# Kernel optimization log

Hardware: AMD Instinct MI355X
Metric: run time of the kernel (lower is better)

Reference implementation:

```python
import jax, jax.numpy as jnp
import numpy as np

N, NFEAT, NHID, NCLASS = 10000, 512, 64, 10
ALPHA = 0.2


def setup_inputs() -> dict:
    key = jax.random.key(0)
    ks = jax.random.split(key, 8)
    x = jax.random.normal(ks[0], (N, NFEAT), dtype=jnp.float32)
    adj1 = jax.random.uniform(ks[1], (N, N), dtype=jnp.float32) / N  # row-normalized-ish
    adj2 = jax.random.uniform(ks[2], (N, N), dtype=jnp.float32) / N
    # GraphConvolution params (glorot-ish scale)
    W1 = jax.random.normal(ks[3], (NFEAT, NHID), dtype=jnp.float32) * (1.0 / np.sqrt(NFEAT))
    b1 = jnp.zeros((NHID,), dtype=jnp.float32)
    W2 = jax.random.normal(ks[4], (NFEAT, NHID), dtype=jnp.float32) * (1.0 / np.sqrt(NFEAT))
    b2 = jnp.zeros((NHID,), dtype=jnp.float32)
    attn_w = jax.random.normal(ks[5], (NHID, 1), dtype=jnp.float32) * (1.0 / np.sqrt(NHID))
    cluster = jax.random.normal(ks[6], (NCLASS, NHID), dtype=jnp.float32)
    return {"x": x, "adj1": adj1, "adj2": adj2, "W1": W1, "b1": b1,
            "W2": W2, "b2": b2, "attn_w": attn_w, "cluster": cluster}


def reference(x, adj1, adj2, W1, b1, W2, b2, attn_w, cluster):
    # Two GCN branches: output = adj @ (x @ W) + b
    emb1 = adj1 @ (x @ W1) + b1  # [N, H]
    emb2 = adj2 @ (x @ W2) + b2  # [N, H]
    z = jnp.stack([emb1, emb2], axis=1)            # [N, 2, H]
    # tiny 2-way attention fusion
    w = z @ attn_w                                  # [N, 2, 1]
    beta = jax.nn.softmax(w, axis=1)                # softmax over the 2 views
    emb = jnp.sum(beta * z, axis=1)                 # [N, H]
    # DEC cluster assignment (faithful to the original, including the
    # second power and the /2, which the row-normalization cancels)
    d2 = jnp.sum((emb[:, None, :] - cluster[None, :, :]) ** 2, axis=2)  # [N, K]
    q = 1.0 / (1.0 + d2 / ALPHA)
    q = q ** ((ALPHA + 1.0) / 2.0)
    q = q ** (ALPHA + 1.0) / 2.0
    q = q / jnp.sum(q, axis=1, keepdims=True)
    return emb, q
```

## Files before the change

kernel.cpp:

```cpp
#include <hip/hip_runtime.h>
#include <math.h>

#define NROWS 10000
#define FEAT  512
#define NHID  64
#define NCLS  10
#define YT_STRIDE 10240
#define KB_PAD 320
#define TK    128
#define NSPLIT 8
#define TILES_PER_SPLIT 10

typedef __attribute__((ext_vector_type(8))) short short8;
typedef __attribute__((ext_vector_type(4))) float f32x4;

__device__ __forceinline__ short f2bf(float f) {
  union { float f; unsigned u; } v; v.f = f;
  unsigned r = v.u + 0x7fffu + ((v.u >> 16) & 1u);
  return (short)(r >> 16);
}

__device__ __forceinline__ float wsum64(float v) {
#pragma unroll
  for (int off = 32; off > 0; off >>= 1) v += __shfl_xor(v, off, 64);
  return v;
}

__device__ __forceinline__ void gload16(const void* g, void* l) {
  __builtin_amdgcn_global_load_lds(
      (const __attribute__((address_space(1))) unsigned int*)g,
      (__attribute__((address_space(3))) unsigned int*)l, 16, 0, 0);
}

__global__ __launch_bounds__(256) void prep_w(const float* __restrict__ W1,
                                              const float* __restrict__ W2,
                                              unsigned short* __restrict__ Wt1,
                                              unsigned short* __restrict__ Wt2) {
  int i = blockIdx.x * 256 + threadIdx.x;
  if (i >= FEAT * NHID) return;
  int k = i >> 6, h = i & 63;
  Wt1[h * FEAT + k] = (unsigned short)f2bf(W1[i]);
  Wt2[h * FEAT + k] = (unsigned short)f2bf(W2[i]);
}

__global__ __launch_bounds__(256) void gemm_xw(const float* __restrict__ x,
                                               const unsigned short* __restrict__ Wt1,
                                               const unsigned short* __restrict__ Wt2,
                                               unsigned short* __restrict__ Yt1,
                                               unsigned short* __restrict__ Yt2) {
  const int lane = threadIdx.x & 63;
  const int wave = threadIdx.x >> 6;
  const int job = blockIdx.x * 4 + wave;
  if (job >= 1250) return;
  const int br = (job >= 625) ? 1 : 0;
  const int tile = job - 625 * br;
  const unsigned short* Wt = br ? Wt2 : Wt1;
  unsigned short* Yt       = br ? Yt2 : Yt1;
  const int rowbase = tile * 16;
  const int r16 = lane & 15, g = lane >> 4, ga = g * 8;

  const float* arow = x + (size_t)(rowbase + r16) * FEAT + ga;
  const unsigned short* bp = Wt + (size_t)r16 * FEAT + ga;

  f32x4 acc[4];
#pragma unroll
  for (int t = 0; t < 4; ++t) acc[t] = (f32x4){0.f, 0.f, 0.f, 0.f};

#pragma unroll
  for (int kb = 0; kb < FEAT / 32; ++kb) {
    const int k0 = kb * 32;
    const f32x4* ap = (const f32x4*)(arow + k0);
    f32x4 a0 = ap[0], a1 = ap[1];
    short8 af;
    af[0] = f2bf(a0[0]); af[1] = f2bf(a0[1]); af[2] = f2bf(a0[2]); af[3] = f2bf(a0[3]);
    af[4] = f2bf(a1[0]); af[5] = f2bf(a1[1]); af[6] = f2bf(a1[2]); af[7] = f2bf(a1[3]);
#pragma unroll
    for (int t = 0; t < 4; ++t) {
      short8 bf = *(const short8*)(bp + (size_t)t * 16 * FEAT + k0);
      acc[t] = __builtin_amdgcn_mfma_f32_16x16x32_bf16(af, bf, acc[t], 0, 0, 0);
    }
  }
  const int sw = (r16 & 7) << 3;
#pragma unroll
  for (int t = 0; t < 4; ++t)
#pragma unroll
    for (int rr = 0; rr < 4; ++rr) {
      const int col = t * 16 + r16;
      const int row = rowbase + g * 4 + rr;
      Yt[(size_t)col * YT_STRIDE + (row ^ sw)] = (unsigned short)f2bf(acc[t][rr]);
    }
}

__global__ __launch_bounds__(256, 4) void gemm_adj(const float* __restrict__ adj1,
                                                   const float* __restrict__ adj2,
                                                   const unsigned short* __restrict__ Yt1,
                                                   const unsigned short* __restrict__ Yt2,
                                                   float* __restrict__ Ep) {
  __shared__ __attribute__((aligned(16))) float Asm[2][32 * TK];

  const int sp = blockIdx.y;
  const int br = blockIdx.z;
  const float* adj         = br ? adj2 : adj1;
  const unsigned short* Yt = br ? Yt2 : Yt1;
  float* E = Ep + (size_t)(br * NSPLIT + sp) * NROWS * NHID;
  const int k_base = sp * (TILES_PER_SPLIT * TK);
  const int blockrow = blockIdx.x * 32;

  const int lane = threadIdx.x & 63;
  const int wave = threadIdx.x >> 6;

  const int l32 = lane >> 5;
  const int a_lin = (lane & 31) * 4;

  const int wr = wave >> 1, wc = wave & 1;
  const int r16 = lane & 15, g = lane >> 4;
  const int arow_t = wr * 16 + r16;
  const int aswz = (arow_t & 7) << 2;
  const int swb = (r16 & 7) << 3;

  const int colL = wc * 32 + r16;
  const unsigned short* ytL = Yt + (size_t)colL * YT_STRIDE;
  const unsigned short* ytH = ytL + (size_t)16 * YT_STRIDE;

  f32x4 accL = (f32x4){0.f, 0.f, 0.f, 0.f};
  f32x4 accH = accL;

#define STAGE_A(tt) { const int k0s = k_base + (tt) * TK; const int bufs = (tt) & 1; \
    _Pragma("unroll")                                                                 \
    for (int j = 0; j < 4; ++j) {                                                     \
      const int rt = wave * 8 + 2 * j + l32;                                          \
      const int gr = min(blockrow + rt, NROWS - 1);                                   \
      const int fsrc = a_lin ^ ((rt & 7) << 2);                                       \
      const float* asrc = adj + (size_t)gr * NROWS + min(k0s + fsrc, NROWS - 4);      \
      gload16(asrc, &Asm[bufs][(wave * 8 + 2 * j) * TK]);                             \
    } }

#define BLOAD(tt) { const int k0b = k_base + (tt) * TK;                               \
    _Pragma("unroll")                                                                 \
    for (int s = 0; s < 4; ++s) {                                                     \
      const int off = k0b + ((s * 32 + g * 8) ^ swb);                                 \
      BL[s] = *(const short8*)(ytL + off);                                            \
      BH[s] = *(const short8*)(ytH + off);                                            \
    } }

#define COMPUTE(tt) { const int bufc = (tt) & 1;                                      \
    const float* abase = &Asm[bufc][arow_t * TK];                                     \
    _Pragma("unroll")                                                                 \
    for (int s = 0; s < 4; ++s) {                                                     \
      const int kx = s * 32 + g * 8;                                                  \
      f32x4 a0 = *(const f32x4*)(abase + (kx ^ aswz));                                \
      f32x4 a1 = *(const f32x4*)(abase + ((kx + 4) ^ aswz));                          \
      short8 af;                                                                      \
      af[0] = f2bf(a0[0]); af[1] = f2bf(a0[1]); af[2] = f2bf(a0[2]); af[3] = f2bf(a0[3]); \
      af[4] = f2bf(a1[0]); af[5] = f2bf(a1[1]); af[6] = f2bf(a1[2]); af[7] = f2bf(a1[3]); \
      accL = __builtin_amdgcn_mfma_f32_16x16x32_bf16(af, BL[s], accL, 0, 0, 0);       \
      accH = __builtin_amdgcn_mfma_f32_16x16x32_bf16(af, BH[s], accH, 0, 0, 0);       \
    } }

  STAGE_A(0);
#pragma unroll 1
  for (int t = 0; t < TILES_PER_SPLIT - 1; ++t) {
    short8 BL[4], BH[4];
    BLOAD(t);
    __builtin_amdgcn_sched_barrier(0);
    asm volatile("" ::: "memory");
    STAGE_A(t + 1);
    asm volatile("s_waitcnt vmcnt(4)" ::: "memory");
    __builtin_amdgcn_sched_barrier(0);
    __builtin_amdgcn_s_barrier();
    __builtin_amdgcn_sched_barrier(0);
    COMPUTE(t);
    __builtin_amdgcn_s_barrier();
  }
  {
    short8 BL[4], BH[4];
    BLOAD(TILES_PER_SPLIT - 1);
    asm volatile("s_waitcnt vmcnt(0)" ::: "memory");
    __builtin_amdgcn_sched_barrier(0);
    __builtin_amdgcn_s_barrier();
    __builtin_amdgcn_sched_barrier(0);
    COMPUTE(TILES_PER_SPLIT - 1);
  }
#undef STAGE_A
#undef BLOAD
#undef COMPUTE

#pragma unroll
  for (int rr = 0; rr < 4; ++rr) {
    const int grow = blockrow + wr * 16 + g * 4 + rr;
    if (grow < NROWS) {
      float* e = E + (size_t)grow * NHID + wc * 32 + r16;
      e[0]  = accL[rr];
      e[16] = accH[rr];
    }
  }
}

__global__ __launch_bounds__(256) void gemm_adj_dyn(const float* __restrict__ adj1,
                                                    const float* __restrict__ adj2,
                                                    const unsigned short* __restrict__ Yt1,
                                                    const unsigned short* __restrict__ Yt2,
                                                    float* __restrict__ Ep,
                                                    int nsplit, int chunk) {
  const int sp = blockIdx.y;
  const int br = blockIdx.z;
  const float* adj          = br ? adj2 : adj1;
  const unsigned short* Yt  = br ? Yt2 : Yt1;
  float* E = Ep + (size_t)(br * nsplit + sp) * NROWS * NHID;

  const int kb_begin = sp * chunk;
  const int kb_end   = min(kb_begin + chunk, KB_PAD);

  const int lane = threadIdx.x & 63;
  const int wave = threadIdx.x >> 6;
  const int rowbase = blockIdx.x * 64 + wave * 16;
  if (rowbase >= NROWS) return;
  const int r = lane & 15;
  const int g = lane >> 4;
  const int ga = g * 8;
  const int sw = (r & 7) << 3;

  const float* arow = adj + (size_t)(rowbase + r) * NROWS;

  f32x4 acc0 = (f32x4){0.f, 0.f, 0.f, 0.f};
  f32x4 acc1 = acc0, acc2 = acc0, acc3 = acc0;

#pragma unroll 4
  for (int kb = kb_begin; kb < kb_end; ++kb) {
    const int k0 = kb * 32;
    const int kc = min(k0 + ga, 9992);
    const int ks = (k0 + ga) ^ sw;
    const f32x4* ap = (const f32x4*)(arow + kc);
    f32x4 a0 = ap[0], a1 = ap[1];
    short8 af;
    af[0] = f2bf(a0[0]); af[1] = f2bf(a0[1]); af[2] = f2bf(a0[2]); af[3] = f2bf(a0[3]);
    af[4] = f2bf(a1[0]); af[5] = f2bf(a1[1]); af[6] = f2bf(a1[2]); af[7] = f2bf(a1[3]);
    short8 bf0 = *(const short8*)(Yt + (size_t)(0 * 16 + r) * YT_STRIDE + ks);
    short8 bf1 = *(const short8*)(Yt + (size_t)(1 * 16 + r) * YT_STRIDE + ks);
    short8 bf2 = *(const short8*)(Yt + (size_t)(2 * 16 + r) * YT_STRIDE + ks);
    short8 bf3 = *(const short8*)(Yt + (size_t)(3 * 16 + r) * YT_STRIDE + ks);
    acc0 = __builtin_amdgcn_mfma_f32_16x16x32_bf16(af, bf0, acc0, 0, 0, 0);
    acc1 = __builtin_amdgcn_mfma_f32_16x16x32_bf16(af, bf1, acc1, 0, 0, 0);
    acc2 = __builtin_amdgcn_mfma_f32_16x16x32_bf16(af, bf2, acc2, 0, 0, 0);
    acc3 = __builtin_amdgcn_mfma_f32_16x16x32_bf16(af, bf3, acc3, 0, 0, 0);
  }

  const size_t ebase = (size_t)(rowbase + g * 4) * NHID + r;
#pragma unroll
  for (int rr = 0; rr < 4; ++rr) {
    E[ebase + (size_t)rr * NHID +  0] = acc0[rr];
    E[ebase + (size_t)rr * NHID + 16] = acc1[rr];
    E[ebase + (size_t)rr * NHID + 32] = acc2[rr];
    E[ebase + (size_t)rr * NHID + 48] = acc3[rr];
  }
}

__global__ __launch_bounds__(256) void fuse(const float* __restrict__ Ep,
                                            int nsplit,
                                            const float* __restrict__ b1,
                                            const float* __restrict__ b2,
                                            const float* __restrict__ aw,
                                            const float* __restrict__ cl,
                                            float* __restrict__ out) {
  const int lane = threadIdx.x & 63;
  const int wave = threadIdx.x >> 6;
  const int row = blockIdx.x * 4 + wave;
  if (row >= NROWS) return;

  const size_t off = (size_t)row * NHID + lane;
  const size_t bstride = (size_t)nsplit * NROWS * NHID;
  float e1 = b1[lane], e2 = b2[lane];
  for (int s = 0; s < nsplit; ++s) {
    e1 += Ep[(size_t)s * NROWS * NHID + off];
    e2 += Ep[bstride + (size_t)s * NROWS * NHID + off];
  }

  float a = aw[lane];
  float w1 = wsum64(e1 * a);
  float w2 = wsum64(e2 * a);
  float m = fmaxf(w1, w2);
  float x1 = expf(w1 - m), x2 = expf(w2 - m);
  float inv = 1.0f / (x1 + x2);
  float emb = (x1 * e1 + x2 * e2) * inv;
  out[off] = emb;

  float myq = 0.f, qs = 0.f;
#pragma unroll
  for (int c = 0; c < NCLS; ++c) {
    float d = emb - cl[c * NHID + lane];
    float s = wsum64(d * d);
    float t = exp2f(-0.72f * log2f(fmaf(5.0f, s, 1.0f)));
    qs += t;
    if (lane == c) myq = t;
  }
  if (lane < NCLS) out[(size_t)NROWS * NHID + (size_t)row * NCLS + lane] = myq / qs;
}

extern "C" void kernel_launch(void* const* d_in, const int* in_sizes, int n_in,
                              void* d_out, int out_size, void* d_ws, size_t ws_size,
                              hipStream_t stream) {
  const float* x    = (const float*)d_in[0];
  const float* adj1 = (const float*)d_in[1];
  const float* adj2 = (const float*)d_in[2];
  const float* W1   = (const float*)d_in[3];
  const float* b1   = (const float*)d_in[4];
  const float* W2   = (const float*)d_in[5];
  const float* b2   = (const float*)d_in[6];
  const float* aw   = (const float*)d_in[7];
  const float* cl   = (const float*)d_in[8];
  float* out = (float*)d_out;

  char* ws = (char*)d_ws;
  unsigned short* Yt1 = (unsigned short*)(ws + 0);
  unsigned short* Yt2 = (unsigned short*)(ws + 1310720);
  unsigned short* Wt1 = (unsigned short*)(ws + 2621440);
  unsigned short* Wt2 = (unsigned short*)(ws + 2686976);
  float* Ep           = (float*)(ws + 2752512);

  const size_t fixed = 2752512;
  const size_t per_split = 2ull * NROWS * NHID * 4ull;
  const bool static_ok = ws_size >= fixed + (size_t)NSPLIT * per_split;

  hipMemsetAsync(Yt1, 0, 2 * 1310720, stream);
  prep_w<<<dim3(128), dim3(256), 0, stream>>>(W1, W2, Wt1, Wt2);
  gemm_xw<<<dim3(313), dim3(256), 0, stream>>>(x, Wt1, Wt2, Yt1, Yt2);

  if (static_ok) {
    gemm_adj<<<dim3(313, NSPLIT, 2), dim3(256), 0, stream>>>(adj1, adj2, Yt1, Yt2, Ep);
    fuse<<<dim3(2500), dim3(256), 0, stream>>>(Ep, NSPLIT, b1, b2, aw, cl, out);
  } else {
    int nsplit = 1;
    if (ws_size > fixed + per_split) {
      size_t s = (ws_size - fixed) / per_split;
      nsplit = (int)(s < 8 ? s : 8);
      if (nsplit < 1) nsplit = 1;
    }
    const int chunk = (KB_PAD + nsplit - 1) / nsplit;
    gemm_adj_dyn<<<dim3(157, nsplit, 2), dim3(256), 0, stream>>>(adj1, adj2, Yt1, Yt2,
                                                                 Ep, nsplit, chunk);
    fuse<<<dim3(2500), dim3(256), 0, stream>>>(Ep, nsplit, b1, b2, aw, cl, out);
  }
}
```

Measured before the change: 270.1 us.

## Stage Y tiles through LDS and use 64-row blocks in adjacency GEMM

The adjacency GEMM now computes 64 rows per block with a 2x2 MFMA tile per wave, where it used 32 rows. The bf16 Y^T operand is staged into LDS alongside adj with async global-to-LDS loads, replacing per-wave direct global loads. K tile shrinks to 64 and split-K drops to 5 with 32 tiles each, which cuts redundant reads of Y and the number of partial sums the fuse kernel must reduce. Grid size halves and LDS per block grows, so fewer blocks fit per CU (launch bounds lowered to 3), which may reduce latency hiding for the bandwidth-bound adj stream.

```diff
diff --git a/kernel.cpp b/kernel.cpp
--- a/kernel.cpp
+++ b/kernel.cpp
@@ -7,9 +7,9 @@
 #define NCLS  10
 #define YT_STRIDE 10240
 #define KB_PAD 320
-#define TK    128
-#define NSPLIT 8
-#define TILES_PER_SPLIT 10
+#define TK    64
+#define NSPLIT 5
+#define NT    32
 
 typedef __attribute__((ext_vector_type(8))) short short8;
 typedef __attribute__((ext_vector_type(4))) float f32x4;
@@ -91,107 +91,113 @@
     }
 }
 
-__global__ __launch_bounds__(256, 4) void gemm_adj(const float* __restrict__ adj1,
+__global__ __launch_bounds__(256, 3) void gemm_adj(const float* __restrict__ adj1,
                                                    const float* __restrict__ adj2,
                                                    const unsigned short* __restrict__ Yt1,
                                                    const unsigned short* __restrict__ Yt2,
                                                    float* __restrict__ Ep) {
-  __shared__ __attribute__((aligned(16))) float Asm[2][32 * TK];
+  __shared__ __attribute__((aligned(16))) float          Asm[2][64 * TK];
+  __shared__ __attribute__((aligned(16))) unsigned short Bsm[2][64 * TK];
 
   const int sp = blockIdx.y;
   const int br = blockIdx.z;
   const float* adj         = br ? adj2 : adj1;
   const unsigned short* Yt = br ? Yt2 : Yt1;
   float* E = Ep + (size_t)(br * NSPLIT + sp) * NROWS * NHID;
-  const int k_base = sp * (TILES_PER_SPLIT * TK);
-  const int blockrow = blockIdx.x * 32;
+  const int k_base = sp * (NT * TK);
+  const int blockrow = blockIdx.x * 64;
 
   const int lane = threadIdx.x & 63;
   const int wave = threadIdx.x >> 6;
 
-  const int l32 = lane >> 5;
-  const int a_lin = (lane & 31) * 4;
+  const int a_rt_l = (lane >> 4);
+  const int a_gran = (lane & 15) * 4;
+  const int b_cl = lane >> 3;
+  const int b_el = (lane & 7) * 8;
 
   const int wr = wave >> 1, wc = wave & 1;
   const int r16 = lane & 15, g = lane >> 4;
-  const int arow_t = wr * 16 + r16;
-  const int aswz = (arow_t & 7) << 2;
-  const int swb = (r16 & 7) << 3;
-
-  const int colL = wc * 32 + r16;
-  const unsigned short* ytL = Yt + (size_t)colL * YT_STRIDE;
-  const unsigned short* ytH = ytL + (size_t)16 * YT_STRIDE;
-
-  f32x4 accL = (f32x4){0.f, 0.f, 0.f, 0.f};
-  f32x4 accH = accL;
-
-#define STAGE_A(tt) { const int k0s = k_base + (tt) * TK; const int bufs = (tt) & 1; \
+  const int aswz = (r16 & 7) << 2;
+  const int swb  = (r16 & 7) << 3;
+
+  f32x4 acc00 = (f32x4){0.f, 0.f, 0.f, 0.f};
+  f32x4 acc01 = acc00, acc10 = acc00, acc11 = acc00;
+
+#define STAGE(tt) { const int k0s = k_base + (tt) * TK; const int bufs = (tt) & 1;   \
     _Pragma("unroll")                                                                 \
     for (int j = 0; j < 4; ++j) {                                                     \
-      const int rt = wave * 8 + 2 * j + l32;                                          \
+      const int rt = wave * 16 + j * 4 + a_rt_l;                                      \
       const int gr = min(blockrow + rt, NROWS - 1);                                   \
-      const int fsrc = a_lin ^ ((rt & 7) << 2);                                       \
+      const int fsrc = a_gran ^ ((rt & 7) << 2);                                      \
       const float* asrc = adj + (size_t)gr * NROWS + min(k0s + fsrc, NROWS - 4);      \
-      gload16(asrc, &Asm[bufs][(wave * 8 + 2 * j) * TK]);                             \
+      gload16(asrc, &Asm[bufs][(wave * 16 + j * 4) * TK]);                            \
+    }                                                                                 \
+    _Pragma("unroll")                                                                 \
+    for (int j = 0; j < 2; ++j) {                                                     \
+      const int c0 = wave * 16 + j * 8;                                               \
+      const unsigned short* bsrc =                                                    \
+          Yt + (size_t)(c0 + b_cl) * YT_STRIDE + (k0s + b_el);                        \
+      gload16(bsrc, &Bsm[bufs][c0 * TK]);                                             \
     } }
 
-#define BLOAD(tt) { const int k0b = k_base + (tt) * TK;                               \
+#define COMPUTE(tt) { const int bufc = (tt) & 1;                                      \
     _Pragma("unroll")                                                                 \
-    for (int s = 0; s < 4; ++s) {                                                     \
-      const int off = k0b + ((s * 32 + g * 8) ^ swb);                                 \
-      BL[s] = *(const short8*)(ytL + off);                                            \
-      BH[s] = *(const short8*)(ytH + off);                                            \
+    for (int ks = 0; ks < 2; ++ks) {                                                  \
+      const int kx = ks * 32 + g * 8;                                                 \
+      const float* ab0 = &Asm[bufc][(wr * 32 + r16) * TK];                            \
+      const float* ab1 = &Asm[bufc][(wr * 32 + 16 + r16) * TK];                       \
+      f32x4 a00 = *(const f32x4*)(ab0 + (kx ^ aswz));                                 \
+      f32x4 a01 = *(const f32x4*)(ab0 + ((kx + 4) ^ aswz));                           \
+      f32x4 a10 = *(const f32x4*)(ab1 + (kx ^ aswz));                                 \
+      f32x4 a11 = *(const f32x4*)(ab1 + ((kx + 4) ^ aswz));                           \
+      short8 b0 = *(const short8*)&Bsm[bufc][(wc * 32 + r16) * TK + (kx ^ swb)];      \
+      short8 b1 = *(const short8*)&Bsm[bufc][(wc * 32 + 16 + r16) * TK + (kx ^ swb)]; \
+      short8 af0, af1;                                                                \
+      af0[0] = f2bf(a00[0]); af0[1] = f2bf(a00[1]); af0[2] = f2bf(a00[2]);            \
+      af0[3] = f2bf(a00[3]); af0[4] = f2bf(a01[0]); af0[5] = f2bf(a01[1]);            \
+      af0[6] = f2bf(a01[2]); af0[7] = f2bf(a01[3]);                                   \
+      af1[0] = f2bf(a10[0]); af1[1] = f2bf(a10[1]); af1[2] = f2bf(a10[2]);            \
+      af1[3] = f2bf(a10[3]); af1[4] = f2bf(a11[0]); af1[5] = f2bf(a11[1]);            \
+      af1[6] = f2bf(a11[2]); af1[7] = f2bf(a11[3]);                                   \
+      acc00 = __builtin_amdgcn_mfma_f32_16x16x32_bf16(af0, b0, acc00, 0, 0, 0);       \
+      acc01 = __builtin_amdgcn_mfma_f32_16x16x32_bf16(af0, b1, acc01, 0, 0, 0);       \
+      acc10 = __builtin_amdgcn_mfma_f32_16x16x32_bf16(af1, b0, acc10, 0, 0, 0);       \
+      acc11 = __builtin_amdgcn_mfma_f32_16x16x32_bf16(af1, b1, acc11, 0, 0, 0);       \
     } }
 
-#define COMPUTE(tt) { const int bufc = (tt) & 1;                                      \
-    const float* abase = &Asm[bufc][arow_t * TK];                                     \
-    _Pragma("unroll")                                                                 \
-    for (int s = 0; s < 4; ++s) {                                                     \
-      const int kx = s * 32 + g * 8;                                                  \
-      f32x4 a0 = *(const f32x4*)(abase + (kx ^ aswz));                                \
-      f32x4 a1 = *(const f32x4*)(abase + ((kx + 4) ^ aswz));                          \
-      short8 af;                                                                      \
-      af[0] = f2bf(a0[0]); af[1] = f2bf(a0[1]); af[2] = f2bf(a0[2]); af[3] = f2bf(a0[3]); \
-      af[4] = f2bf(a1[0]); af[5] = f2bf(a1[1]); af[6] = f2bf(a1[2]); af[7] = f2bf(a1[3]); \
-      accL = __builtin_amdgcn_mfma_f32_16x16x32_bf16(af, BL[s], accL, 0, 0, 0);       \
-      accH = __builtin_amdgcn_mfma_f32_16x16x32_bf16(af, BH[s], accH, 0, 0, 0);       \
-    } }
-
-  STAGE_A(0);
-#pragma unroll 1
-  for (int t = 0; t < TILES_PER_SPLIT - 1; ++t) {
-    short8 BL[4], BH[4];
-    BLOAD(t);
-    __builtin_amdgcn_sched_barrier(0);
-    asm volatile("" ::: "memory");
-    STAGE_A(t + 1);
-    asm volatile("s_waitcnt vmcnt(4)" ::: "memory");
+  STAGE(0);
+#pragma unroll 2
+  for (int t = 0; t < NT - 1; ++t) {
+    STAGE(t + 1);
+    asm volatile("s_waitcnt vmcnt(6)" ::: "memory");
     __builtin_amdgcn_sched_barrier(0);
     __builtin_amdgcn_s_barrier();
     __builtin_amdgcn_sched_barrier(0);
     COMPUTE(t);
     __builtin_amdgcn_s_barrier();
   }
-  {
-    short8 BL[4], BH[4];
-    BLOAD(TILES_PER_SPLIT - 1);
-    asm volatile("s_waitcnt vmcnt(0)" ::: "memory");
-    __builtin_amdgcn_sched_barrier(0);
-    __builtin_amdgcn_s_barrier();
-    __builtin_amdgcn_sched_barrier(0);
-    COMPUTE(TILES_PER_SPLIT - 1);
-  }
-#undef STAGE_A
-#undef BLOAD
+  asm volatile("s_waitcnt vmcnt(0)" ::: "memory");
+  __builtin_amdgcn_sched_barrier(0);
+  __builtin_amdgcn_s_barrier();
+  __builtin_amdgcn_sched_barrier(0);
+  COMPUTE(NT - 1);
+#undef STAGE
 #undef COMPUTE
 
 #pragma unroll
   for (int rr = 0; rr < 4; ++rr) {
-    const int grow = blockrow + wr * 16 + g * 4 + rr;
-    if (grow < NROWS) {
-      float* e = E + (size_t)grow * NHID + wc * 32 + r16;
-      e[0]  = accL[rr];
-      e[16] = accH[rr];
+    const int grow0 = blockrow + wr * 32 + g * 4 + rr;
+    const int grow1 = grow0 + 16;
+    const int col   = wc * 32 + r16;
+    if (grow0 < NROWS) {
+      float* e = E + (size_t)grow0 * NHID + col;
+      e[0]  = acc00[rr];
+      e[16] = acc01[rr];
+    }
+    if (grow1 < NROWS) {
+      float* e = E + (size_t)grow1 * NHID + col;
+      e[0]  = acc10[rr];
+      e[16] = acc11[rr];
     }
   }
 }
@@ -326,13 +332,13 @@
   gemm_xw<<<dim3(313), dim3(256), 0, stream>>>(x, Wt1, Wt2, Yt1, Yt2);
 
   if (static_ok) {
-    gemm_adj<<<dim3(313, NSPLIT, 2), dim3(256), 0, stream>>>(adj1, adj2, Yt1, Yt2, Ep);
+    gemm_adj<<<dim3(157, NSPLIT, 2), dim3(256), 0, stream>>>(adj1, adj2, Yt1, Yt2, Ep);
     fuse<<<dim3(2500), dim3(256), 0, stream>>>(Ep, NSPLIT, b1, b2, aw, cl, out);
   } else {
     int nsplit = 1;
     if (ws_size > fixed + per_split) {
       size_t s = (ws_size - fixed) / per_split;
-      nsplit = (int)(s < 8 ? s : 8);
+      nsplit = (int)(s < 5 ? s : 5);
       if (nsplit < 1) nsplit = 1;
     }
     const int chunk = (KB_PAD + nsplit - 1) / nsplit;
```

Measured after the change: 232.9 us. -13.8%, faster.
